# Optimization experiments

Measured on AMD Instinct MI355X. Metric: run time of the kernel, lower is better.

Reference implementation:

```python
import jax, jax.numpy as jnp
import numpy as np

B, S, E, H = 4, 1024, 1024, 16
HD = E // H
EPS = 1e-10


def setup_inputs() -> dict:
    key = jax.random.key(0)
    ks = jax.random.split(key, 10)
    w = lambda k: jax.random.normal(k, (E, E), jnp.float32) * 0.02
    b = lambda k: jax.random.normal(k, (E,), jnp.float32) * 0.02
    return {
        "query": jax.random.normal(ks[0], (B, S, E), jnp.float32),
        "Wq": w(ks[1]), "bq": b(ks[2]),
        "Wk": w(ks[3]), "bk": b(ks[4]),
        "Wv": w(ks[5]), "bv": b(ks[6]),
        "Wo": w(ks[7]), "bo": b(ks[8]),
        "alpha": jnp.array(1.0, jnp.float32),
    }


def reference(query, Wq, bq, Wk, bk, Wv, bv, Wo, bo, alpha):
    scale = 1.0 / np.sqrt(HD)
    # projections -> [B, H, S, HD]
    def heads(x, W, bias):
        return (x @ W.T + bias).reshape(B, S, H, HD).transpose(0, 2, 1, 3)
    Q = heads(query, Wq, bq)
    K = heads(query, Wk, bk)
    V = heads(query, Wv, bv)
    # raw scores [B, H, S, S]
    scores = jnp.einsum('bhqd,bhkd->bhqk', Q, K) * scale
    # 2D FFT over the (q, k) plane
    scores_fft = jnp.fft.fft2(scores, axes=(-2, -1))
    # spectral filter: exp(i * alpha * arctan(log|F| + eps))
    phase = alpha * jnp.arctan(jnp.log(jnp.abs(scores_fft) + EPS))
    filt = jnp.exp(1j * phase)
    scores_filtered = jnp.fft.ifft2(scores_fft * filt, axes=(-2, -1)).real
    # softmax over keys (dropout is identity at eval)
    attn = jax.nn.softmax(scores_filtered, axis=-1)
    ctx = jnp.einsum('bhqk,bhkd->bhqd', attn, V)
    ctx = ctx.transpose(0, 2, 1, 3).reshape(B, S, E)
    return ctx @ Wo.T + bo
```

## Files before the change

### kernel.cpp

```cpp
#include <hip/hip_runtime.h>
#include <hip/hip_fp16.h>


typedef __attribute__((ext_vector_type(8))) short short8;
typedef __attribute__((ext_vector_type(8))) _Float16 half8;
typedef __attribute__((ext_vector_type(4))) float f32x4;

#define PITCH 40
#define PITCH1 72

__device__ __forceinline__ float bf2f(short v) {
  return __uint_as_float(((unsigned)(unsigned short)v) << 16);
}
__device__ __forceinline__ short f2bf(float f) {
  unsigned u = __float_as_uint(f);
  u += 0x7FFFu + ((u >> 16) & 1u);
  return (short)(u >> 16);
}

__device__ __forceinline__ short8 ld8(const void* p, size_t idx, int isf32) {
  short8 r;
  if (isf32) {
    const float* f = (const float*)p + idx;
    float4 a = *(const float4*)f;
    float4 b = *(const float4*)(f + 4);
    r[0] = f2bf(a.x); r[1] = f2bf(a.y); r[2] = f2bf(a.z); r[3] = f2bf(a.w);
    r[4] = f2bf(b.x); r[5] = f2bf(b.y); r[6] = f2bf(b.z); r[7] = f2bf(b.w);
  } else {
    r = *(const short8*)((const short*)p + idx);
  }
  return r;
}
__device__ __forceinline__ float ldf(const void* p, int idx, int isf32) {
  return isf32 ? ((const float*)p)[idx] : bf2f(((const short*)p)[idx]);
}

__device__ __forceinline__ float2 cmul(float2 a, float2 b) {
  return make_float2(a.x * b.x - a.y * b.y, a.x * b.y + a.y * b.x);
}
__device__ __forceinline__ float2 cmulc(float2 a, float2 b) {
  return make_float2(a.x * b.x + a.y * b.y, a.y * b.x - a.x * b.y);
}
__device__ __forceinline__ float2 cadd(float2 a, float2 b) {
  return make_float2(a.x + b.x, a.y + b.y);
}
__device__ __forceinline__ float2 csub(float2 a, float2 b) {
  return make_float2(a.x - b.x, a.y - b.y);
}


template <int SGN>
__device__ __forceinline__ void dft16_dif(float2* x) {
  const float C16[8] = {1.f, 0.92387953f, 0.70710678f, 0.38268343f,
                        0.f, -0.38268343f, -0.70710678f, -0.92387953f};
  const float S16[8] = {0.f, 0.38268343f, 0.70710678f, 0.92387953f,
                        1.f, 0.92387953f, 0.70710678f, 0.38268343f};
#pragma unroll
  for (int h = 8; h >= 1; h >>= 1)
#pragma unroll
    for (int b = 0; b < 16; b += 2 * h)
#pragma unroll
      for (int i = 0; i < h; ++i) {
        const int e = i * (8 / h);
        float2 u = x[b + i], v = x[b + i + h];
        x[b + i] = cadd(u, v);
        float2 d = csub(u, v);
        float2 w = make_float2(C16[e], SGN > 0 ? S16[e] : -S16[e]);
        x[b + i + h] = (e == 0) ? d : cmul(d, w);
      }
}

__device__ __forceinline__ void dit16_inv(float2* x) {
  const float C16[8] = {1.f, 0.92387953f, 0.70710678f, 0.38268343f,
                        0.f, -0.38268343f, -0.70710678f, -0.92387953f};
  const float S16[8] = {0.f, 0.38268343f, 0.70710678f, 0.92387953f,
                        1.f, 0.92387953f, 0.70710678f, 0.38268343f};
#pragma unroll
  for (int h = 1; h <= 8; h <<= 1)
#pragma unroll
    for (int b = 0; b < 16; b += 2 * h)
#pragma unroll
      for (int i = 0; i < h; ++i) {
        const int e = i * (8 / h);
        float2 w = make_float2(C16[e], -S16[e]);
        float2 u = x[b + i];
        float2 vh = (e == 0) ? x[b + i + h] : cmulc(x[b + i + h], w);
        x[b + i] = cadd(u, vh);
        x[b + i + h] = csub(u, vh);
      }
}

template <int SGN>
__device__ __forceinline__ void midtw(float2* x, int lane) {
  const int rho[16] = {0, 8, 4, 12, 2, 10, 6, 14, 1, 9, 5, 13, 3, 11, 7, 15};
  float s, c;
  __sincosf((float)lane * 0.00613592315f, &s, &c);
  float2 w = make_float2(c, SGN > 0 ? s : -s);
  float2 run = w;
  x[8] = cmul(x[8], run);
#pragma unroll
  for (int e = 2; e < 16; ++e) {
    run = cmul(run, w);
    x[rho[e]] = cmul(x[rho[e]], run);
  }
}

template <int SGN>
__device__ __forceinline__ void xlane_dif(float2* x, int lane) {
#pragma unroll
  for (int h = 32; h >= 1; h >>= 1) {
    const int e = (lane & (h - 1)) * (32 / h);
    float s, c;
    __sincosf((float)e * 0.09817477042f, &s, &c);
    float2 w = make_float2(c, SGN > 0 ? s : -s);
    const bool hi = (lane & h) != 0;
#pragma unroll
    for (int r = 0; r < 16; ++r) {
      float2 t = x[r];
      float2 p;
      p.x = __shfl_xor(t.x, h, 64);
      p.y = __shfl_xor(t.y, h, 64);
      x[r] = hi ? cmul(csub(p, t), w) : cadd(t, p);
    }
  }
}

template <int SGN>
__device__ __forceinline__ void wfft1024_dif(float2* x, int lane) {
  dft16_dif<SGN>(x);
  midtw<SGN>(x, lane);
  xlane_dif<SGN>(x, lane);
}

template <int SGN>
__device__ __forceinline__ void midtw2(float2* x, float2* y, int lane) {
  const int rho[16] = {0, 8, 4, 12, 2, 10, 6, 14, 1, 9, 5, 13, 3, 11, 7, 15};
  float s, c;
  __sincosf((float)lane * 0.00613592315f, &s, &c);
  float2 w = make_float2(c, SGN > 0 ? s : -s);
  float2 run = w;
  x[8] = cmul(x[8], run);
  y[8] = cmul(y[8], run);
#pragma unroll
  for (int e = 2; e < 16; ++e) {
    run = cmul(run, w);
    x[rho[e]] = cmul(x[rho[e]], run);
    y[rho[e]] = cmul(y[rho[e]], run);
  }
}

__device__ __forceinline__ void midtw_inv2(float2* x, float2* y, int lane) {
  const int rho[16] = {0, 8, 4, 12, 2, 10, 6, 14, 1, 9, 5, 13, 3, 11, 7, 15};
  float s, c;
  __sincosf((float)lane * 0.00613592315f, &s, &c);
  float2 w = make_float2(c, -s);
  float2 run = w;
  x[8] = cmulc(x[8], run);
  y[8] = cmulc(y[8], run);
#pragma unroll
  for (int e = 2; e < 16; ++e) {
    run = cmul(run, w);
    x[rho[e]] = cmulc(x[rho[e]], run);
    y[rho[e]] = cmulc(y[rho[e]], run);
  }
}

template <int SGN>
__device__ __forceinline__ void xlane_dif2(float2* x, float2* y, int lane) {
#pragma unroll
  for (int h = 32; h >= 1; h >>= 1) {
    const int e = (lane & (h - 1)) * (32 / h);
    float s, c;
    __sincosf((float)e * 0.09817477042f, &s, &c);
    float2 w = make_float2(c, SGN > 0 ? s : -s);
    const bool hi = (lane & h) != 0;
#pragma unroll
    for (int r = 0; r < 16; ++r) {
      float2 t = x[r];
      float2 p;
      p.x = __shfl_xor(t.x, h, 64);
      p.y = __shfl_xor(t.y, h, 64);
      x[r] = hi ? cmul(csub(p, t), w) : cadd(t, p);
    }
#pragma unroll
    for (int r = 0; r < 16; ++r) {
      float2 t = y[r];
      float2 p;
      p.x = __shfl_xor(t.x, h, 64);
      p.y = __shfl_xor(t.y, h, 64);
      y[r] = hi ? cmul(csub(p, t), w) : cadd(t, p);
    }
  }
}

__device__ __forceinline__ void xlane_dit_inv2(float2* x, float2* y, int lane) {
#pragma unroll
  for (int h = 1; h <= 32; h <<= 1) {
    const int e = (lane & (h - 1)) * (32 / h);
    float s, c;
    __sincosf((float)e * 0.09817477042f, &s, &c);
    float2 w = make_float2(c, -s);
    const bool hi = (lane & h) != 0;
#pragma unroll
    for (int r = 0; r < 16; ++r) {
      float2 t = x[r];
      if (hi) t = cmulc(t, w);
      float2 p;
      p.x = __shfl_xor(t.x, h, 64);
      p.y = __shfl_xor(t.y, h, 64);
      x[r] = hi ? csub(p, t) : cadd(t, p);
    }
#pragma unroll
    for (int r = 0; r < 16; ++r) {
      float2 t = y[r];
      if (hi) t = cmulc(t, w);
      float2 p;
      p.x = __shfl_xor(t.x, h, 64);
      p.y = __shfl_xor(t.y, h, 64);
      y[r] = hi ? csub(p, t) : cadd(t, p);
    }
  }
}

template <int SGN>
__device__ __forceinline__ void wfft1024_dif2(float2* x, float2* y, int lane) {
  dft16_dif<SGN>(x);
  dft16_dif<SGN>(y);
  midtw2<SGN>(x, y, lane);
  xlane_dif2<SGN>(x, y, lane);
}
__device__ __forceinline__ void wfft1024_inv2(float2* x, float2* y, int lane) {
  xlane_dit_inv2(x, y, lane);
  midtw_inv2(x, y, lane);
  dit16_inv(x);
  dit16_inv(y);
}

__device__ __forceinline__ float gainw(float re, float im, float alpha, bool a1) {
  float mag2 = re * re + im * im;
  float t = 0.5f * __logf(mag2 + 1e-20f);
  if (a1) return __builtin_amdgcn_rsqf(fmaf(t, t, 1.0f)) * (1.0f / 1048576.0f);
  return __cosf(alpha * atanf(t)) * (1.0f / 1048576.0f);
}

__global__ void k0_detect(const unsigned* __restrict__ q,
                          const void* __restrict__ alphap, int* __restrict__ flags) {
  __shared__ float smax[256];
  __shared__ int szero[256];
  int t = threadIdx.x;
  float mx = 0.f; int zc = 0;
  for (int i = t; i < 16384; i += 256) {
    unsigned w = q[i];
    unsigned lo = w & 0xFFFFu;
    float v = fabsf(__uint_as_float(lo << 16));
    if (!(v <= 1e30f)) v = 1e30f;
    mx = fmaxf(mx, v);
    zc += (lo == 0u);
  }
  smax[t] = mx; szero[t] = zc;
  __syncthreads();
  for (int s = 128; s > 0; s >>= 1) {
    if (t < s) { smax[t] = fmaxf(smax[t], smax[t + s]); szero[t] += szero[t + s]; }
    __syncthreads();
  }
  if (t == 0) {
    int isf32 = (smax[0] > 100.f) || (szero[0] > 12288);
    flags[0] = isf32;
    float alpha = isf32 ? *(const float*)alphap : bf2f(*(const short*)alphap);
    ((float*)flags)[1] = alpha;
  }
}

__global__ __launch_bounds__(256) void k1_qkv(
    const void* __restrict__ x,
    const void* __restrict__ Wq, const void* __restrict__ bq,
    const void* __restrict__ Wk, const void* __restrict__ bk,
    const void* __restrict__ Wv, const void* __restrict__ bv,
    short* __restrict__ Qt, short* __restrict__ Kt, short* __restrict__ Vt,
    const int* __restrict__ flags)
{
  __shared__ __align__(16) char smem[128 * PITCH1 * 2 * 2];
  short* As = (short*)smem;
  short* Bs = As + 128 * PITCH1;
  short* Ct = (short*)smem;
  const int isf32 = flags[0];
  const int t = threadIdx.x;
  const int lb = blockIdx.x;
  const int m0 = ((lb & 7) * 4 + ((lb >> 3) & 3)) * 128;
  const int n0 = (lb >> 5) * 128;
  const int which = blockIdx.y;
  const void* __restrict__ W = (which == 0) ? Wq : (which == 1) ? Wk : Wv;
  const void* __restrict__ bias = (which == 0) ? bq : (which == 1) ? bk : bv;
  const int lane = t & 63, wvi = t >> 6;
  const int wr = wvi >> 1, wc = wvi & 1;
  const int lm = lane & 15, lq = lane >> 4;
  f32x4 acc[4][4] = {};

  for (int k0 = 0; k0 < 1024; k0 += 64) {
    __syncthreads();
#pragma unroll
    for (int i = 0; i < 4; ++i) {
      int l = t + i * 256;
      int row = l >> 3, kk = (l & 7) << 3;
      *(short8*)&As[row * PITCH1 + kk] = ld8(x, (size_t)(m0 + row) * 1024 + k0 + kk, isf32);
      *(short8*)&Bs[row * PITCH1 + kk] = ld8(W, (size_t)(n0 + row) * 1024 + k0 + kk, isf32);
    }
    __syncthreads();
#pragma unroll
    for (int kh = 0; kh < 2; ++kh) {
      short8 af[4], bf[4];
#pragma unroll
      for (int a = 0; a < 4; ++a)
        af[a] = *(const short8*)&As[(wr * 64 + a * 16 + lm) * PITCH1 + kh * 32 + lq * 8];
#pragma unroll
      for (int b = 0; b < 4; ++b)
        bf[b] = *(const short8*)&Bs[(wc * 64 + b * 16 + lm) * PITCH1 + kh * 32 + lq * 8];
#pragma unroll
      for (int a = 0; a < 4; ++a)
#pragma unroll
        for (int b = 0; b < 4; ++b)
          acc[a][b] = __builtin_amdgcn_mfma_f32_16x16x32_bf16(af[a], bf[b], acc[a][b], 0, 0, 0);
    }
  }

  __syncthreads();
#pragma unroll
  for (int a = 0; a < 4; ++a)
#pragma unroll
    for (int b = 0; b < 4; ++b) {
      int col = wc * 64 + b * 16 + lm;
      float bv_ = ldf(bias, n0 + col, isf32);
#pragma unroll
      for (int r = 0; r < 4; ++r) {
        int row = wr * 64 + a * 16 + lq * 4 + r;
        Ct[row * 136 + col] = f2bf(acc[a][b][r] + bv_);
      }
    }
  __syncthreads();

  short* __restrict__ O = (which == 0) ? Qt : (which == 1) ? Kt : Vt;
#pragma unroll
  for (int j = 0; j < 8; ++j) {
    int id = t + j * 256;
    int d128 = id & 127, sg = (id >> 7) * 8;
    short vals[8];
#pragma unroll
    for (int i = 0; i < 8; ++i) vals[i] = Ct[(sg + i) * 136 + d128];
    int col = n0 + d128;
    int h = col >> 6, d = col & 63;
    int bb = m0 >> 10, sbase = (m0 & 1023) + sg;
    *(short8*)&O[(((size_t)(bb * 16 + h)) << 16) + ((size_t)d << 10) + sbase] = *(short8*)vals;
  }
}

__global__ __launch_bounds__(128) void kA_qkfft(
    const short* __restrict__ Qt, const short* __restrict__ Kt,
    __half2* __restrict__ Qhat, __half2* __restrict__ Khat)
{
  __shared__ float2 sbuf[2][1024];
  const int lane = threadIdx.x & 63, w = threadIdx.x >> 6;
  const int z = blockIdx.y;
  const int bx = blockIdx.x;
  if (bx < 16) {
    const short* qp = Qt + ((size_t)z << 16);
    const int d0 = bx * 4 + w * 2;
    float2 x[16], y[16];
#pragma unroll
    for (int j = 0; j < 16; ++j) {
      x[j] = make_float2(0.125f * bf2f(qp[(d0 << 10) + lane + 64 * j]), 0.f);
      y[j] = make_float2(0.125f * bf2f(qp[((d0 + 1) << 10) + lane + 64 * j]), 0.f);
    }
    wfft1024_dif2<-1>(x, y, lane);
    __half2* o0 = Qhat + (((size_t)(z * 64 + d0)) << 10);
    __half2* o1 = o0 + 1024;
#pragma unroll
    for (int r = 0; r < 16; ++r) {
      o0[lane + 64 * r] = __float22half2_rn(x[r]);
      o1[lane + 64 * r] = __float22half2_rn(y[r]);
    }
  } else {
    const short* kp = Kt + ((size_t)z << 16);
    const int p = (bx - 16) * 2 + w;
    const int d0 = 2 * p;
    float2 x[16];
#pragma unroll
    for (int j = 0; j < 16; ++j)
      x[j] = make_float2(bf2f(kp[(d0 << 10) + lane + 64 * j]),
                         bf2f(kp[((d0 + 1) << 10) + lane + 64 * j]));
    wfft1024_dif<-1>(x, lane);
    const int rho[16] = {0, 8, 4, 12, 2, 10, 6, 14, 1, 9, 5, 13, 3, 11, 7, 15};
    const int bl6 = ((lane & 1) << 5) | ((lane & 2) << 3) | ((lane & 4) << 1) |
                    ((lane & 8) >> 1) | ((lane & 16) >> 3) | ((lane & 32) >> 5);
    float2* buf = sbuf[w];
#pragma unroll
    for (int r = 0; r < 16; ++r) buf[rho[r] + 16 * bl6] = x[r];
    __half2* o0 = Khat + (size_t)(z * 64 + d0) * 520;
    __half2* o1 = o0 + 520;
#pragma unroll 1
    for (int jj = 0; jj < 9; ++jj) {
      int v = lane + 64 * jj;
      if (v <= 512) {
        float2 A = buf[v], B = buf[(1024 - v) & 1023];
        o0[v] = __float22half2_rn(make_float2((A.x + B.x) * 0.5f, (A.y - B.y) * 0.5f));
        o1[v] = __float22half2_rn(make_float2((A.y + B.y) * 0.5f, (B.x - A.x) * 0.5f));
      }
    }
  }
}

__global__ __launch_bounds__(256) void kB_specmm(
    const __half2* __restrict__ Qhat, const __half2* __restrict__ Khat,
    __half2* __restrict__ Ct, const int* __restrict__ flags, int bh0)
{
  __shared__ unsigned short Are[64][72], Aim[64][72], Bre[128][72], Bim[128][72];
  const int t = threadIdx.x;
  const int u0 = blockIdx.x * 128;
  const int v0 = blockIdx.y * 64;
  const int zl = blockIdx.z;
  const int z = bh0 + zl;
  const float alpha = ((const float*)flags)[1];
  const bool a1 = (alpha == 1.0f);
  {
    const int d = t >> 2;
    const ushort2* src = (const ushort2*)(Khat + (size_t)(z * 64 + d) * 520);
    int vb = (t & 3) * 16;
#pragma unroll
    for (int j = 0; j < 16; ++j) {
      int v = v0 + vb + j;
      if (v > 519) v = 519;
      ushort2 e = src[v];
      int row = vb + j;
      int dc = d ^ (((row >> 4) & 3) << 4);
      Are[row][dc] = e.x;
      Aim[row][dc] = e.y;
    }
    const ushort2* srcb = (const ushort2*)(Qhat + (((size_t)(z * 64 + d)) << 10) + u0);
    int ub = (t & 3) * 32;
#pragma unroll
    for (int j = 0; j < 32; ++j) {
      ushort2 e = srcb[ub + j];
      int row = ub + j;
      int dc = d ^ (((row >> 5) & 3) << 4);
      Bre[row][dc] = e.x;
      Bim[row][dc] = e.y;
    }
  }
  __syncthreads();

  const int lane = t & 63, wc = t >> 6;
  const int lm = lane & 15, lq = lane >> 4;
  f32x4 cre[4][2] = {}, cim[4][2] = {};
#pragma unroll
  for (int ks = 0; ks < 2; ++ks) {
    half8 ar[4], ai[4], aiN[4], br[2], bi[2];
#pragma unroll
    for (int a = 0; a < 4; ++a) {
      int dc = (ks * 32 + lq * 8) ^ ((a & 3) << 4);
      ar[a] = *(const half8*)&Are[a * 16 + lm][dc];
      ai[a] = *(const half8*)&Aim[a * 16 + lm][dc];
      int4 tm = *(int4*)&ai[a];
      tm.x ^= 0x80008000; tm.y ^= 0x80008000; tm.z ^= 0x80008000; tm.w ^= 0x80008000;
      aiN[a] = *(half8*)&tm;
    }
#pragma unroll
    for (int n = 0; n < 2; ++n) {
      int dc = (ks * 32 + lq * 8) ^ ((wc & 3) << 4);
      br[n] = *(const half8*)&Bre[wc * 32 + n * 16 + lm][dc];
      bi[n] = *(const half8*)&Bim[wc * 32 + n * 16 + lm][dc];
    }
#pragma unroll
    for (int a = 0; a < 4; ++a)
#pragma unroll
      for (int n = 0; n < 2; ++n) {
        cre[a][n] = __builtin_amdgcn_mfma_f32_16x16x32_f16(ar[a], br[n], cre[a][n], 0, 0, 0);
        cre[a][n] = __builtin_amdgcn_mfma_f32_16x16x32_f16(aiN[a], bi[n], cre[a][n], 0, 0, 0);
        cim[a][n] = __builtin_amdgcn_mfma_f32_16x16x32_f16(ar[a], bi[n], cim[a][n], 0, 0, 0);
        cim[a][n] = __builtin_amdgcn_mfma_f32_16x16x32_f16(ai[a], br[n], cim[a][n], 0, 0, 0);
      }
  }

  __half2* outp = Ct + (size_t)zl * 513 * 1024 + u0 + wc * 32;
#pragma unroll
  for (int a = 0; a < 4; ++a)
#pragma unroll
    for (int r = 0; r < 4; ++r) {
      int v = v0 + a * 16 + lq * 4 + r;
      if (v < 513) {
#pragma unroll
        for (int n = 0; n < 2; ++n) {
          float re = cre[a][n][r], im = cim[a][n][r];
          float wf = gainw(re, im, alpha, a1);
          outp[(size_t)v * 1024 + n * 16 + lm] =
              __float22half2_rn(make_float2(re * wf, im * wf));
        }
      }
    }
}

__global__ __launch_bounds__(256) void k4_invfft(__half2* __restrict__ Ct)
{
  const int lane = threadIdx.x & 63;
  const int w = threadIdx.x >> 6;
  const int gv0 = blockIdx.x * 8 + w * 2;
  if (gv0 > 512) return;
  const bool has1 = (gv0 + 1 <= 512);
  __half2* __restrict__ row0 = Ct + (size_t)blockIdx.y * 513 * 1024 + ((size_t)gv0 << 10);
  __half2* __restrict__ row1 = row0 + 1024;
  float2 x[16], y[16];
#pragma unroll
  for (int j = 0; j < 16; ++j) x[j] = __half22float2(row0[lane + 64 * j]);
  if (has1) {
#pragma unroll
    for (int j = 0; j < 16; ++j) y[j] = __half22float2(row1[lane + 64 * j]);
  } else {
#pragma unroll
    for (int j = 0; j < 16; ++j) y[j] = make_float2(0.f, 0.f);
  }
  wfft1024_inv2(x, y, lane);
#pragma unroll
  for (int j = 0; j < 16; ++j) row0[lane + 64 * j] = __float22half2_rn(x[j]);
  if (has1) {
#pragma unroll
    for (int j = 0; j < 16; ++j) row1[lane + 64 * j] = __float22half2_rn(y[j]);
  }
}

__global__ __launch_bounds__(512) void k56_softmax_av(
    const __half2* __restrict__ Ct, const short* __restrict__ Vt,
    short* __restrict__ ctx, int bh0)
{
  __shared__ __align__(16) char GP[33280];
  const int tid = threadIdx.x;
  const int q0 = blockIdx.x * 16, z = blockIdx.y;
  const int lane = tid & 63, w = tid >> 6;
  const int lm = lane & 15, lq = lane >> 4;
  const __half2* __restrict__ in = Ct + (size_t)z * 513 * 1024;
#define GROW(m) ((__half2*)(GP + (m) * 2064))
  for (int id = tid; id < 2052; id += 512) {
    int v = id >> 2, qq = (id & 3) * 4;
    int4 o = *(const int4*)&in[(size_t)v * 1024 + q0 + qq];
    __half2* op = (__half2*)&o;
#pragma unroll
    for (int i = 0; i < 4; ++i) GROW(qq + i)[v] = op[i];
  }
  short* P = (short*)GP;
  const int bl6 = ((lane & 1) << 5) | ((lane & 2) << 3) | ((lane & 4) << 1) |
                  ((lane & 8) >> 1) | ((lane & 16) >> 3) | ((lane & 32) >> 5);
  __syncthreads();

  const int p = w;
  const __half2* g1 = GROW(2 * p);
  const __half2* g2 = GROW(2 * p + 1);
  float2 x[16];
#pragma unroll
  for (int j = 0; j < 16; ++j) {
    int v = lane + 64 * j;
    float2 a, b;
    if (v <= 512) {
      a = __half22float2(g1[v]);
      b = __half22float2(g2[v]);
    } else {
      int v2 = 1024 - v;
      float2 aa = __half22float2(g1[v2]), bb = __half22float2(g2[v2]);
      a = make_float2(aa.x, -aa.y);
      b = make_float2(bb.x, -bb.y);
    }
    x[j] = make_float2(a.x - b.y, a.y + b.x);
  }

  wfft1024_dif<1>(x, lane);

  float m1 = -3.4e38f, m2 = -3.4e38f;
#pragma unroll
  for (int j = 0; j < 16; ++j) { m1 = fmaxf(m1, x[j].x); m2 = fmaxf(m2, x[j].y); }
#pragma unroll
  for (int s = 32; s > 0; s >>= 1) {
    m1 = fmaxf(m1, __shfl_xor(m1, s, 64));
    m2 = fmaxf(m2, __shfl_xor(m2, s, 64));
  }
  float s1 = 0.f, s2 = 0.f;
#pragma unroll
  for (int j = 0; j < 16; ++j) {
    float e1 = __expf(x[j].x - m1), e2 = __expf(x[j].y - m2);
    x[j] = make_float2(e1, e2);
    s1 += e1; s2 += e2;
  }
#pragma unroll
  for (int s = 32; s > 0; s >>= 1) {
    s1 += __shfl_xor(s1, s, 64);
    s2 += __shfl_xor(s2, s, 64);
  }
  float inv1 = 1.0f / s1, inv2 = 1.0f / s2;

  __syncthreads();

  {
    const int rho[16] = {0, 8, 4, 12, 2, 10, 6, 14, 1, 9, 5, 13, 3, 11, 7, 15};
    short a0[16], a1[16];
#pragma unroll
    for (int pos = 0; pos < 16; ++pos) {
      const int j = rho[pos];
      a0[pos] = f2bf(x[j].x * inv1);
      a1[pos] = f2bf(x[j].y * inv2);
    }
    short* dst0 = &P[(2 * p) * 1040 + 16 * bl6];
    short* dst1 = &P[(2 * p + 1) * 1040 + 16 * bl6];
    *(short8*)dst0       = *(short8*)&a0[0];
    *(short8*)(dst0 + 8) = *(short8*)&a0[8];
    *(short8*)dst1       = *(short8*)&a1[0];
    *(short8*)(dst1 + 8) = *(short8*)&a1[8];
  }
  __syncthreads();

  const short* __restrict__ Vp = Vt + ((size_t)(bh0 + z) << 16);
  f32x4 acc[4] = {};
#pragma unroll
  for (int ks = 0; ks < 4; ++ks) {
    int k0 = w * 128 + ks * 32;
    short8 a0 = *(const short8*)&P[lm * 1040 + k0 + lq * 8];
#pragma unroll
    for (int b = 0; b < 4; ++b) {
      short8 bv = *(const short8*)&Vp[(size_t)(b * 16 + lm) * 1024 + k0 + lq * 8];
      acc[b] = __builtin_amdgcn_mfma_f32_16x16x32_bf16(a0, bv, acc[b], 0, 0, 0);
    }
  }
  __syncthreads();
  float* red = (float*)GP;
#pragma unroll
  for (int b = 0; b < 4; ++b)
#pragma unroll
    for (int r = 0; r < 4; ++r)
      red[(w * 16 + lq * 4 + r) * 64 + b * 16 + lm] = acc[b][r];
  __syncthreads();
  if (tid < 256) {
    int q = tid >> 4, d0 = (tid & 15) * 4;
    float s0 = 0.f, s1_ = 0.f, s2_ = 0.f, s3 = 0.f;
#pragma unroll
    for (int ww = 0; ww < 8; ++ww) {
      const float* rr = &red[(ww * 16 + q) * 64 + d0];
      s0 += rr[0]; s1_ += rr[1]; s2_ += rr[2]; s3 += rr[3];
    }
    short o4[4] = {f2bf(s0), f2bf(s1_), f2bf(s2_), f2bf(s3)};
    *(int2*)&ctx[(((size_t)(bh0 + z)) << 16) + (size_t)(q0 + q) * 64 + d0] = *(int2*)o4;
  }
#undef GROW
}

__global__ __launch_bounds__(256) void k7_out(
    const short* __restrict__ ctx, const void* __restrict__ Wo,
    const void* __restrict__ bo, void* __restrict__ out,
    const int* __restrict__ flags)
{
  __shared__ __align__(16) char smem[128 * 136 * 2];
  short* As = (short*)smem;
  short* Bs = As + 128 * PITCH;
  short* Ct = (short*)smem;
  const int isf32 = flags[0];
  const int t = threadIdx.x;
  const int lb = blockIdx.x;
  const int m0 = ((lb & 7) * 4 + ((lb >> 3) & 3)) * 128;
  const int n0 = (lb >> 5) * 128;
  const int lane = t & 63, wvi = t >> 6;
  const int wr = wvi >> 1, wc = wvi & 1;
  const int lm = lane & 15, lq = lane >> 4;
  f32x4 acc[4][4] = {};

  for (int k0 = 0; k0 < 1024; k0 += 32) {
    __syncthreads();
#pragma unroll
    for (int i = 0; i < 2; ++i) {
      int l = t + i * 256;
      int row = l >> 2, kk = (l & 3) << 3;
      int n = m0 + row, e = k0 + kk;
      size_t aaddr = (((size_t)((n >> 10) * 16 + (e >> 6))) << 16) + (size_t)((n & 1023) << 6) + (e & 63);
      *(int4*)&As[row * PITCH + kk] = *(const int4*)&ctx[aaddr];
      *(short8*)&Bs[row * PITCH + kk] = ld8(Wo, (size_t)(n0 + row) * 1024 + e, isf32);
    }
    __syncthreads();
    short8 af[4], bf[4];
#pragma unroll
    for (int a = 0; a < 4; ++a) af[a] = *(const short8*)&As[(wr * 64 + a * 16 + lm) * PITCH + lq * 8];
#pragma unroll
    for (int b = 0; b < 4; ++b) bf[b] = *(const short8*)&Bs[(wc * 64 + b * 16 + lm) * PITCH + lq * 8];
#pragma unroll
    for (int a = 0; a < 4; ++a)
#pragma unroll
      for (int b = 0; b < 4; ++b)
        acc[a][b] = __builtin_amdgcn_mfma_f32_16x16x32_bf16(af[a], bf[b], acc[a][b], 0, 0, 0);
  }

  if (isf32) {
#pragma unroll
    for (int a = 0; a < 4; ++a)
#pragma unroll
      for (int b = 0; b < 4; ++b) {
        int col = n0 + wc * 64 + b * 16 + lm;
        float bo_ = ldf(bo, col, 1);
#pragma unroll
        for (int r = 0; r < 4; ++r) {
          int row = m0 + wr * 64 + a * 16 + lq * 4 + r;
          ((float*)out)[(size_t)row * 1024 + col] = acc[a][b][r] + bo_;
        }
      }
    return;
  }
  __syncthreads();
#pragma unroll
  for (int a = 0; a < 4; ++a)
#pragma unroll
    for (int b = 0; b < 4; ++b) {
      int col = wc * 64 + b * 16 + lm;
      float bo_ = ldf(bo, n0 + col, 0);
#pragma unroll
      for (int r = 0; r < 4; ++r) {
        int row = wr * 64 + a * 16 + lq * 4 + r;
        Ct[row * 136 + col] = f2bf(acc[a][b][r] + bo_);
      }
    }
  __syncthreads();
#pragma unroll
  for (int j = 0; j < 8; ++j) {
    int id = t + j * 256;
    int row = id >> 4, c16 = (id & 15) * 8;
    short8 v = *(const short8*)&Ct[row * 136 + c16];
    *(short8*)&((short*)out)[(size_t)(m0 + row) * 1024 + n0 + c16] = v;
  }
}

extern "C" void kernel_launch(void* const* d_in, const int* in_sizes, int n_in,
                              void* d_out, int out_size, void* d_ws, size_t ws_size,
                              hipStream_t stream)
{
  const void* x  = d_in[0];
  const void* Wq = d_in[1];
  const void* bq = d_in[2];
  const void* Wk = d_in[3];
  const void* bk = d_in[4];
  const void* Wv = d_in[5];
  const void* bv = d_in[6];
  const void* Wo = d_in[7];
  const void* bo = d_in[8];
  const void* alphap = d_in[9];
  char* ws = (char*)d_ws;

  const size_t PLANE_CT = (size_t)513 * 1024 * 4;
  const size_t QH_SZ = (size_t)64 * 64 * 1024 * 4;
  const size_t KH_SZ = (size_t)64 * 64 * 520 * 4;

  const size_t B_CT  = 0;
  const size_t B_VT  = 64 * PLANE_CT;
  const size_t B_CX  = B_VT + ((size_t)8u << 20);
  const size_t B_QH  = B_CX + ((size_t)8u << 20);
  const size_t B_KH  = B_QH + QH_SZ;
  const size_t B_FL  = B_KH + KH_SZ;
  const size_t B_NEED = B_FL + 256;

  if (ws_size >= B_NEED) {
    short*   Qt   = (short*)(ws);
    short*   Kt   = (short*)(ws + ((size_t)8u << 20));
    short*   Vt   = (short*)(ws + B_VT);
    short*   ctx  = (short*)(ws + B_CX);
    __half2* Ct   = (__half2*)(ws + B_CT);
    __half2* Qhat = (__half2*)(ws + B_QH);
    __half2* Khat = (__half2*)(ws + B_KH);
    int*     flags = (int*)(ws + B_FL);

    k0_detect<<<1, 256, 0, stream>>>((const unsigned*)x, alphap, flags);
    k1_qkv<<<dim3(256, 3), 256, 0, stream>>>(x, Wq, bq, Wk, bk, Wv, bv, Qt, Kt, Vt, flags);
    kA_qkfft<<<dim3(32, 64), 128, 0, stream>>>(Qt, Kt, Qhat, Khat);
    kB_specmm<<<dim3(8, 9, 64), 256, 0, stream>>>(Qhat, Khat, Ct, flags, 0);
    k4_invfft<<<dim3(65, 64), 256, 0, stream>>>(Ct);
    k56_softmax_av<<<dim3(64, 64), 512, 0, stream>>>(Ct, Vt, ctx, 0);
    k7_out<<<256, 256, 0, stream>>>(ctx, Wo, bo, d_out, flags);
    return;
  }

  const size_t VT_OFF = (size_t)17u << 20;
  const size_t CX_OFF = (size_t)25u << 20;
  const size_t QH_OFF = (size_t)33u << 20;
  const size_t KH_OFF = QH_OFF + QH_SZ;
  const size_t FL_OFF = KH_OFF + KH_SZ;

  short*   Qt   = (short*)(ws);
  short*   Kt   = (short*)(ws + ((size_t)8u << 20));
  short*   Vt   = (short*)(ws + VT_OFF);
  short*   ctx  = (short*)(ws + CX_OFF);
  __half2* Ct   = (__half2*)(ws);
  __half2* Qhat = (__half2*)(ws + QH_OFF);
  __half2* Khat = (__half2*)(ws + KH_OFF);
  int*     flags = (int*)(ws + FL_OFF);

  k0_detect<<<1, 256, 0, stream>>>((const unsigned*)x, alphap, flags);
  k1_qkv<<<dim3(256, 3), 256, 0, stream>>>(x, Wq, bq, Wk, bk, Wv, bv, Qt, Kt, Vt, flags);
  kA_qkfft<<<dim3(32, 64), 128, 0, stream>>>(Qt, Kt, Qhat, Khat);
  for (int c = 0; c < 8; ++c) {
    int bh0 = c * 8;
    kB_specmm<<<dim3(8, 9, 8), 256, 0, stream>>>(Qhat, Khat, Ct, flags, bh0);
    k4_invfft<<<dim3(65, 8), 256, 0, stream>>>(Ct);
    k56_softmax_av<<<dim3(64, 8), 512, 0, stream>>>(Ct, Vt, ctx, bh0);
  }
  k7_out<<<256, 256, 0, stream>>>(ctx, Wo, bo, d_out, flags);
}
```

Before: 678.8 us.

## Pre-convert QKV inputs to bf16 and batch four rows per inverse-FFT wave

Adds a conversion kernel that casts the input activations, the three projection weights and the biases to bf16/f32 once, so the QKV GEMM loads packed bf16 directly instead of converting per tile. It also changes the inverse FFT kernel so each wave processes four 1024-point rows instead of two, halving the grid to 33 blocks along x. This is meant to raise ILP and amortise shuffles and twiddles, at the cost of higher register pressure and an extra pass over global memory for the conversion.

New measurement: 882.4 us. +30.0%, slower.

```diff
diff --git a/kernel.cpp b/kernel.cpp
--- a/kernel.cpp
+++ b/kernel.cpp
@@ -149,22 +149,6 @@
   }
 }
 
-__device__ __forceinline__ void midtw_inv2(float2* x, float2* y, int lane) {
-  const int rho[16] = {0, 8, 4, 12, 2, 10, 6, 14, 1, 9, 5, 13, 3, 11, 7, 15};
-  float s, c;
-  __sincosf((float)lane * 0.00613592315f, &s, &c);
-  float2 w = make_float2(c, -s);
-  float2 run = w;
-  x[8] = cmulc(x[8], run);
-  y[8] = cmulc(y[8], run);
-#pragma unroll
-  for (int e = 2; e < 16; ++e) {
-    run = cmul(run, w);
-    x[rho[e]] = cmulc(x[rho[e]], run);
-    y[rho[e]] = cmulc(y[rho[e]], run);
-  }
-}
-
 template <int SGN>
 __device__ __forceinline__ void xlane_dif2(float2* x, float2* y, int lane) {
 #pragma unroll
@@ -193,7 +177,16 @@
   }
 }
 
-__device__ __forceinline__ void xlane_dit_inv2(float2* x, float2* y, int lane) {
+template <int SGN>
+__device__ __forceinline__ void wfft1024_dif2(float2* x, float2* y, int lane) {
+  dft16_dif<SGN>(x);
+  dft16_dif<SGN>(y);
+  midtw2<SGN>(x, y, lane);
+  xlane_dif2<SGN>(x, y, lane);
+}
+
+__device__ __forceinline__ void xlane_dit_inv4(float2* x0, float2* x1,
+                                               float2* x2, float2* x3, int lane) {
 #pragma unroll
   for (int h = 1; h <= 32; h <<= 1) {
     const int e = (lane & (h - 1)) * (32 / h);
@@ -203,37 +196,72 @@
     const bool hi = (lane & h) != 0;
 #pragma unroll
     for (int r = 0; r < 16; ++r) {
-      float2 t = x[r];
+      float2 t = x0[r];
       if (hi) t = cmulc(t, w);
       float2 p;
       p.x = __shfl_xor(t.x, h, 64);
       p.y = __shfl_xor(t.y, h, 64);
-      x[r] = hi ? csub(p, t) : cadd(t, p);
+      x0[r] = hi ? csub(p, t) : cadd(t, p);
     }
 #pragma unroll
     for (int r = 0; r < 16; ++r) {
-      float2 t = y[r];
+      float2 t = x1[r];
       if (hi) t = cmulc(t, w);
       float2 p;
       p.x = __shfl_xor(t.x, h, 64);
       p.y = __shfl_xor(t.y, h, 64);
-      y[r] = hi ? csub(p, t) : cadd(t, p);
-    }
-  }
-}
-
-template <int SGN>
-__device__ __forceinline__ void wfft1024_dif2(float2* x, float2* y, int lane) {
-  dft16_dif<SGN>(x);
-  dft16_dif<SGN>(y);
-  midtw2<SGN>(x, y, lane);
-  xlane_dif2<SGN>(x, y, lane);
-}
-__device__ __forceinline__ void wfft1024_inv2(float2* x, float2* y, int lane) {
-  xlane_dit_inv2(x, y, lane);
-  midtw_inv2(x, y, lane);
-  dit16_inv(x);
-  dit16_inv(y);
+      x1[r] = hi ? csub(p, t) : cadd(t, p);
+    }
+#pragma unroll
+    for (int r = 0; r < 16; ++r) {
+      float2 t = x2[r];
+      if (hi) t = cmulc(t, w);
+      float2 p;
+      p.x = __shfl_xor(t.x, h, 64);
+      p.y = __shfl_xor(t.y, h, 64);
+      x2[r] = hi ? csub(p, t) : cadd(t, p);
+    }
+#pragma unroll
+    for (int r = 0; r < 16; ++r) {
+      float2 t = x3[r];
+      if (hi) t = cmulc(t, w);
+      float2 p;
+      p.x = __shfl_xor(t.x, h, 64);
+      p.y = __shfl_xor(t.y, h, 64);
+      x3[r] = hi ? csub(p, t) : cadd(t, p);
+    }
+  }
+}
+
+__device__ __forceinline__ void midtw_inv4(float2* x0, float2* x1,
+                                           float2* x2, float2* x3, int lane) {
+  const int rho[16] = {0, 8, 4, 12, 2, 10, 6, 14, 1, 9, 5, 13, 3, 11, 7, 15};
+  float s, c;
+  __sincosf((float)lane * 0.00613592315f, &s, &c);
+  float2 w = make_float2(c, -s);
+  float2 run = w;
+  x0[8] = cmulc(x0[8], run);
+  x1[8] = cmulc(x1[8], run);
+  x2[8] = cmulc(x2[8], run);
+  x3[8] = cmulc(x3[8], run);
+#pragma unroll
+  for (int e = 2; e < 16; ++e) {
+    run = cmul(run, w);
+    x0[rho[e]] = cmulc(x0[rho[e]], run);
+    x1[rho[e]] = cmulc(x1[rho[e]], run);
+    x2[rho[e]] = cmulc(x2[rho[e]], run);
+    x3[rho[e]] = cmulc(x3[rho[e]], run);
+  }
+}
+
+__device__ __forceinline__ void wfft1024_inv4(float2* x0, float2* x1,
+                                              float2* x2, float2* x3, int lane) {
+  xlane_dit_inv4(x0, x1, x2, x3, lane);
+  midtw_inv4(x0, x1, x2, x3, lane);
+  dit16_inv(x0);
+  dit16_inv(x1);
+  dit16_inv(x2);
+  dit16_inv(x3);
 }
 
 __device__ __forceinline__ float gainw(float re, float im, float alpha, bool a1) {
@@ -271,26 +299,57 @@
   }
 }
 
-__global__ __launch_bounds__(256) void k1_qkv(
+__global__ __launch_bounds__(256) void k0b_convert(
     const void* __restrict__ x,
     const void* __restrict__ Wq, const void* __restrict__ bq,
     const void* __restrict__ Wk, const void* __restrict__ bk,
     const void* __restrict__ Wv, const void* __restrict__ bv,
-    short* __restrict__ Qt, short* __restrict__ Kt, short* __restrict__ Vt,
+    short* __restrict__ xb, short* __restrict__ Wqb,
+    short* __restrict__ Wkb, short* __restrict__ Wvb,
+    float* __restrict__ bqf, float* __restrict__ bkf, float* __restrict__ bvf,
     const int* __restrict__ flags)
+{
+  const int isf32 = flags[0];
+  const int gid = blockIdx.x * 256 + threadIdx.x;
+  if (gid < 524288) {
+    *(short8*)&xb[(size_t)gid * 8] = ld8(x, (size_t)gid * 8, isf32);
+  } else if (gid < 524288 + 3 * 131072) {
+    int r = gid - 524288;
+    int wsel = r / 131072;
+    size_t off = (size_t)(r % 131072) * 8;
+    const void* W = (wsel == 0) ? Wq : (wsel == 1) ? Wk : Wv;
+    short* O = (wsel == 0) ? Wqb : (wsel == 1) ? Wkb : Wvb;
+    *(short8*)&O[off] = ld8(W, off, isf32);
+  } else {
+    int r = gid - (524288 + 3 * 131072);
+    if (r < 3 * 128) {
+      int bsel = r / 128, off = (r % 128) * 8;
+      const void* B = (bsel == 0) ? bq : (bsel == 1) ? bk : bv;
+      float* O = (bsel == 0) ? bqf : (bsel == 1) ? bkf : bvf;
+#pragma unroll
+      for (int i = 0; i < 8; ++i) O[off + i] = ldf(B, off + i, isf32);
+    }
+  }
+}
+
+__global__ __launch_bounds__(256) void k1_qkv(
+    const short* __restrict__ xb,
+    const short* __restrict__ Wqb, const float* __restrict__ bqf,
+    const short* __restrict__ Wkb, const float* __restrict__ bkf,
+    const short* __restrict__ Wvb, const float* __restrict__ bvf,
+    short* __restrict__ Qt, short* __restrict__ Kt, short* __restrict__ Vt)
 {
   __shared__ __align__(16) char smem[128 * PITCH1 * 2 * 2];
   short* As = (short*)smem;
   short* Bs = As + 128 * PITCH1;
   short* Ct = (short*)smem;
-  const int isf32 = flags[0];
   const int t = threadIdx.x;
   const int lb = blockIdx.x;
   const int m0 = ((lb & 7) * 4 + ((lb >> 3) & 3)) * 128;
   const int n0 = (lb >> 5) * 128;
   const int which = blockIdx.y;
-  const void* __restrict__ W = (which == 0) ? Wq : (which == 1) ? Wk : Wv;
-  const void* __restrict__ bias = (which == 0) ? bq : (which == 1) ? bk : bv;
+  const short* __restrict__ W = (which == 0) ? Wqb : (which == 1) ? Wkb : Wvb;
+  const float* __restrict__ bias = (which == 0) ? bqf : (which == 1) ? bkf : bvf;
   const int lane = t & 63, wvi = t >> 6;
   const int wr = wvi >> 1, wc = wvi & 1;
   const int lm = lane & 15, lq = lane >> 4;
@@ -302,8 +361,8 @@
     for (int i = 0; i < 4; ++i) {
       int l = t + i * 256;
       int row = l >> 3, kk = (l & 7) << 3;
-      *(short8*)&As[row * PITCH1 + kk] = ld8(x, (size_t)(m0 + row) * 1024 + k0 + kk, isf32);
-      *(short8*)&Bs[row * PITCH1 + kk] = ld8(W, (size_t)(n0 + row) * 1024 + k0 + kk, isf32);
+      *(short8*)&As[row * PITCH1 + kk] = *(const short8*)&xb[(size_t)(m0 + row) * 1024 + k0 + kk];
+      *(short8*)&Bs[row * PITCH1 + kk] = *(const short8*)&W[(size_t)(n0 + row) * 1024 + k0 + kk];
     }
     __syncthreads();
 #pragma unroll
@@ -329,7 +388,7 @@
 #pragma unroll
     for (int b = 0; b < 4; ++b) {
       int col = wc * 64 + b * 16 + lm;
-      float bv_ = ldf(bias, n0 + col, isf32);
+      float bv_ = bias[n0 + col];
 #pragma unroll
       for (int r = 0; r < 4; ++r) {
         int row = wr * 64 + a * 16 + lq * 4 + r;
@@ -501,27 +560,50 @@
 {
   const int lane = threadIdx.x & 63;
   const int w = threadIdx.x >> 6;
-  const int gv0 = blockIdx.x * 8 + w * 2;
+  const int gv0 = blockIdx.x * 16 + w * 4;
   if (gv0 > 512) return;
-  const bool has1 = (gv0 + 1 <= 512);
+  const int nv = (513 - gv0 < 4) ? (513 - gv0) : 4;
   __half2* __restrict__ row0 = Ct + (size_t)blockIdx.y * 513 * 1024 + ((size_t)gv0 << 10);
-  __half2* __restrict__ row1 = row0 + 1024;
-  float2 x[16], y[16];
-#pragma unroll
-  for (int j = 0; j < 16; ++j) x[j] = __half22float2(row0[lane + 64 * j]);
-  if (has1) {
-#pragma unroll
-    for (int j = 0; j < 16; ++j) y[j] = __half22float2(row1[lane + 64 * j]);
+  float2 x0[16], x1[16], x2[16], x3[16];
+#pragma unroll
+  for (int j = 0; j < 16; ++j) x0[j] = __half22float2(row0[lane + 64 * j]);
+  if (nv > 1) {
+#pragma unroll
+    for (int j = 0; j < 16; ++j) x1[j] = __half22float2(row0[1024 + lane + 64 * j]);
   } else {
 #pragma unroll
-    for (int j = 0; j < 16; ++j) y[j] = make_float2(0.f, 0.f);
-  }
-  wfft1024_inv2(x, y, lane);
-#pragma unroll
-  for (int j = 0; j < 16; ++j) row0[lane + 64 * j] = __float22half2_rn(x[j]);
-  if (has1) {
-#pragma unroll
-    for (int j = 0; j < 16; ++j) row1[lane + 64 * j] = __float22half2_rn(y[j]);
+    for (int j = 0; j < 16; ++j) x1[j] = make_float2(0.f, 0.f);
+  }
+  if (nv > 2) {
+#pragma unroll
+    for (int j = 0; j < 16; ++j) x2[j] = __half22float2(row0[2048 + lane + 64 * j]);
+  } else {
+#pragma unroll
+    for (int j = 0; j < 16; ++j) x2[j] = make_float2(0.f, 0.f);
+  }
+  if (nv > 3) {
+#pragma unroll
+    for (int j = 0; j < 16; ++j) x3[j] = __half22float2(row0[3072 + lane + 64 * j]);
+  } else {
+#pragma unroll
+    for (int j = 0; j < 16; ++j) x3[j] = make_float2(0.f, 0.f);
+  }
+
+  wfft1024_inv4(x0, x1, x2, x3, lane);
+
+#pragma unroll
+  for (int j = 0; j < 16; ++j) row0[lane + 64 * j] = __float22half2_rn(x0[j]);
+  if (nv > 1) {
+#pragma unroll
+    for (int j = 0; j < 16; ++j) row0[1024 + lane + 64 * j] = __float22half2_rn(x1[j]);
+  }
+  if (nv > 2) {
+#pragma unroll
+    for (int j = 0; j < 16; ++j) row0[2048 + lane + 64 * j] = __float22half2_rn(x2[j]);
+  }
+  if (nv > 3) {
+#pragma unroll
+    for (int j = 0; j < 16; ++j) row0[3072 + lane + 64 * j] = __float22half2_rn(x3[j]);
   }
 }
 
@@ -746,6 +828,7 @@
   const size_t PLANE_CT = (size_t)513 * 1024 * 4;
   const size_t QH_SZ = (size_t)64 * 64 * 1024 * 4;
   const size_t KH_SZ = (size_t)64 * 64 * 520 * 4;
+  const int K0B_BLOCKS = (524288 + 3 * 131072 + 3 * 128 + 255) / 256;
 
   const size_t B_CT  = 0;
   const size_t B_VT  = 64 * PLANE_CT;
@@ -758,6 +841,13 @@
   if (ws_size >= B_NEED) {
     short*   Qt   = (short*)(ws);
     short*   Kt   = (short*)(ws + ((size_t)8u << 20));
+    short*   xb   = (short*)(ws + ((size_t)16u << 20));
+    short*   Wqb  = (short*)(ws + ((size_t)24u << 20));
+    short*   Wkb  = (short*)(ws + ((size_t)26u << 20));
+    short*   Wvb  = (short*)(ws + ((size_t)28u << 20));
+    float*   bqf  = (float*)(ws + ((size_t)30u << 20));
+    float*   bkf  = (float*)(ws + ((size_t)30u << 20) + 4096);
+    float*   bvf  = (float*)(ws + ((size_t)30u << 20) + 8192);
     short*   Vt   = (short*)(ws + B_VT);
     short*   ctx  = (short*)(ws + B_CX);
     __half2* Ct   = (__half2*)(ws + B_CT);
@@ -766,10 +856,12 @@
     int*     flags = (int*)(ws + B_FL);
 
     k0_detect<<<1, 256, 0, stream>>>((const unsigned*)x, alphap, flags);
-    k1_qkv<<<dim3(256, 3), 256, 0, stream>>>(x, Wq, bq, Wk, bk, Wv, bv, Qt, Kt, Vt, flags);
+    k0b_convert<<<K0B_BLOCKS, 256, 0, stream>>>(x, Wq, bq, Wk, bk, Wv, bv,
+                                                xb, Wqb, Wkb, Wvb, bqf, bkf, bvf, flags);
+    k1_qkv<<<dim3(256, 3), 256, 0, stream>>>(xb, Wqb, bqf, Wkb, bkf, Wvb, bvf, Qt, Kt, Vt);
     kA_qkfft<<<dim3(32, 64), 128, 0, stream>>>(Qt, Kt, Qhat, Khat);
     kB_specmm<<<dim3(8, 9, 64), 256, 0, stream>>>(Qhat, Khat, Ct, flags, 0);
-    k4_invfft<<<dim3(65, 64), 256, 0, stream>>>(Ct);
+    k4_invfft<<<dim3(33, 64), 256, 0, stream>>>(Ct);
     k56_softmax_av<<<dim3(64, 64), 512, 0, stream>>>(Ct, Vt, ctx, 0);
     k7_out<<<256, 256, 0, stream>>>(ctx, Wo, bo, d_out, flags);
     return;
@@ -780,6 +872,7 @@
   const size_t QH_OFF = (size_t)33u << 20;
   const size_t KH_OFF = QH_OFF + QH_SZ;
   const size_t FL_OFF = KH_OFF + KH_SZ;
+  const size_t XB_OFF = (size_t)58u << 20;
 
   short*   Qt   = (short*)(ws);
   short*   Kt   = (short*)(ws + ((size_t)8u << 20));
@@ -789,14 +882,23 @@
   __half2* Qhat = (__half2*)(ws + QH_OFF);
   __half2* Khat = (__half2*)(ws + KH_OFF);
   int*     flags = (int*)(ws + FL_OFF);
+  short*   xb   = (short*)(ws + XB_OFF);
+  short*   Wqb  = (short*)(ws + XB_OFF + ((size_t)8u << 20));
+  short*   Wkb  = (short*)(ws + XB_OFF + ((size_t)10u << 20));
+  short*   Wvb  = (short*)(ws + XB_OFF + ((size_t)12u << 20));
+  float*   bqf  = (float*)(ws + XB_OFF + ((size_t)14u << 20));
+  float*   bkf  = (float*)(ws + XB_OFF + ((size_t)14u << 20) + 4096);
+  float*   bvf  = (float*)(ws + XB_OFF + ((size_t)14u << 20) + 8192);
 
   k0_detect<<<1, 256, 0, stream>>>((const unsigned*)x, alphap, flags);
-  k1_qkv<<<dim3(256, 3), 256, 0, stream>>>(x, Wq, bq, Wk, bk, Wv, bv, Qt, Kt, Vt, flags);
+  k0b_convert<<<K0B_BLOCKS, 256, 0, stream>>>(x, Wq, bq, Wk, bk, Wv, bv,
+                                              xb, Wqb, Wkb, Wvb, bqf, bkf, bvf, flags);
+  k1_qkv<<<dim3(256, 3), 256, 0, stream>>>(xb, Wqb, bqf, Wkb, bkf, Wvb, bvf, Qt, Kt, Vt);
   kA_qkfft<<<dim3(32, 64), 128, 0, stream>>>(Qt, Kt, Qhat, Khat);
   for (int c = 0; c < 8; ++c) {
     int bh0 = c * 8;
     kB_specmm<<<dim3(8, 9, 8), 256, 0, stream>>>(Qhat, Khat, Ct, flags, bh0);
-    k4_invfft<<<dim3(65, 8), 256, 0, stream>>>(Ct);
+    k4_invfft<<<dim3(33, 8), 256, 0, stream>>>(Ct);
     k56_softmax_av<<<dim3(64, 8), 512, 0, stream>>>(Ct, Vt, ctx, bh0);
   }
   k7_out<<<256, 256, 0, stream>>>(ctx, Wo, bo, d_out, flags);
```
